# Performance work log

Hardware: AMD Instinct MI355X
Metric: run time of the kernel (lower is better)

Reference implementation:

```python
import jax, jax.numpy as jnp
import numpy as np

B, S, D = 2, 2048, 1024
H, HD = 16, 64  # num_heads, head_dim
EPS = 1e-6      # flax LayerNorm default
ROPE_BASE = 10000.0


def _layernorm(x, scale, bias=None, eps=EPS):
    mu = jnp.mean(x, axis=-1, keepdims=True)
    var = jnp.mean(jnp.square(x - mu), axis=-1, keepdims=True)
    y = (x - mu) * jax.lax.rsqrt(var + eps) * scale
    return y + bias if bias is not None else y


def _rotate_half(x):
    x1, x2 = x[..., : x.shape[-1] // 2], x[..., x.shape[-1] // 2 :]
    return jnp.concatenate((-x2, x1), axis=-1)


def _rope_tables(seq_len, head_dim, dtype):
    inv_freq = 1.0 / ROPE_BASE ** (jnp.arange(0, head_dim, 2, dtype=jnp.float32) / head_dim)
    t = jnp.arange(seq_len, dtype=jnp.float32)
    freqs = jnp.einsum('i,j->ij', t, inv_freq)          # [S, HD/2]
    emb = jnp.concatenate((freqs, freqs), axis=-1)      # [S, HD]
    return jnp.cos(emb).astype(dtype), jnp.sin(emb).astype(dtype)


def setup_inputs() -> dict:
    key = jax.random.key(0)
    ks = jax.random.split(key, 4)
    return {
        'x': jax.random.normal(ks[0], (B, S, D), dtype=jnp.float32),
        'w_qkv': jax.random.normal(ks[1], (D, 3 * D), dtype=jnp.float32) * (1.0 / np.sqrt(D)),
        'b_qkv': jnp.zeros((3 * D,), dtype=jnp.float32),
        'w_out': jax.random.normal(ks[2], (D, D), dtype=jnp.float32) * (0.1 / np.sqrt(D)),
        'b_out': jnp.zeros((D,), dtype=jnp.float32),
        'ln_scale': jnp.ones((D,), dtype=jnp.float32),
        'ln_bias': jnp.zeros((D,), dtype=jnp.float32),
        'q_scale': jnp.ones((HD,), dtype=jnp.float32),
        'k_scale': jnp.ones((HD,), dtype=jnp.float32),
    }


def reference(x, w_qkv, b_qkv, w_out, b_out, ln_scale, ln_bias, q_scale, k_scale):
    b, s, d = x.shape
    # input LayerNorm
    xn = _layernorm(x, ln_scale, ln_bias)
    # fused QKV projection
    qkv = xn @ w_qkv + b_qkv                              # [B, S, 3D]
    q, k, v = jnp.split(qkv, 3, axis=-1)
    def to_bhsd(t):
        return t.reshape(b, s, H, HD).transpose(0, 2, 1, 3)
    q, k, v = to_bhsd(q), to_bhsd(k), to_bhsd(v)          # [B, H, S, HD]
    # per-head QK LayerNorm (no bias)
    q = _layernorm(q, q_scale)
    k = _layernorm(k, k_scale)
    # RoPE
    cos, sin = _rope_tables(s, HD, q.dtype)               # [S, HD]
    cos, sin = cos[None, None], sin[None, None]
    q = q * cos + _rotate_half(q) * sin
    k = k * cos + _rotate_half(k) * sin
    # scaled dot-product attention (softmax over key positions)
    scale = 1.0 / np.sqrt(HD)
    scores = jnp.einsum('bhqd,bhkd->bhqk', q, k) * scale  # [B, H, S, S]
    probs = jax.nn.softmax(scores, axis=-1)
    attn = jnp.einsum('bhqk,bhkd->bhqd', probs, v)        # [B, H, S, HD]
    attn = attn.transpose(0, 2, 1, 3).reshape(b, s, d)
    return attn @ w_out + b_out
```

## Files before the change

kernel.cpp:

```cpp
#include <hip/hip_runtime.h>
#include <math.h>

#define BB 2
#define SS 2048
#define DD 1024
#define HH 16
#define HDD 64
static constexpr float EPS = 1e-6f;

typedef __bf16 bf16x8 __attribute__((ext_vector_type(8)));
typedef __bf16 bf16x4 __attribute__((ext_vector_type(4)));
typedef float f32x4 __attribute__((ext_vector_type(4)));
typedef __attribute__((address_space(1))) const unsigned int gas_u32;
typedef __attribute__((address_space(3))) unsigned int las_u32;

__device__ __forceinline__ unsigned short f2bf(float f) {
    unsigned int u = __float_as_uint(f);
    u = (u + 0x7FFFu + ((u >> 16) & 1u)) >> 16;
    return (unsigned short)u;
}

__device__ __forceinline__ uint2 pack4bf(float a, float b, float c, float d) {
    bf16x4 v;
    v[0] = (__bf16)a; v[1] = (__bf16)b; v[2] = (__bf16)c; v[3] = (__bf16)d;
    return *(uint2*)&v;
}

__device__ __forceinline__ void async_ld16(const unsigned short* g, unsigned short* l) {
    __builtin_amdgcn_global_load_lds((gas_u32*)g, (las_u32*)l, 16, 0, 0);
}

__global__ __launch_bounds__(256) void cast_transpose(const float* __restrict__ w,
                                                      unsigned short* __restrict__ wt,
                                                      int K, int N) {
    __shared__ float tile[32][36];
    const int n0 = blockIdx.x * 32;
    const int k0 = blockIdx.y * 32;
    const int t = threadIdx.x;
    const int r = t >> 3;
    const int c = (t & 7) * 4;
    *(float4*)&tile[r][c] = *(const float4*)(w + (size_t)(k0 + r) * N + n0 + c);
    __syncthreads();
    unsigned short o[4];
#pragma unroll
    for (int i = 0; i < 4; i++) o[i] = f2bf(tile[c + i][r]);
    *(uint2*)(wt + (size_t)(n0 + r) * K + k0 + c) = *(uint2*)o;
}

__global__ __launch_bounds__(256) void ln_kernel(const float* __restrict__ x,
                                                 const float* __restrict__ scale,
                                                 const float* __restrict__ bias,
                                                 unsigned short* __restrict__ xn) {
    __shared__ float red[4];
    const int row = blockIdx.x;
    const int t = threadIdx.x;
    const float* xr = x + (size_t)row * DD + t * 4;

    float4 v = *(const float4*)xr;
    float s = v.x + v.y + v.z + v.w;
#pragma unroll
    for (int o = 32; o; o >>= 1) s += __shfl_xor(s, o);
    if ((t & 63) == 0) red[t >> 6] = s;
    __syncthreads();
    const float mu = (red[0] + red[1] + red[2] + red[3]) * (1.f / DD);

    float4 d = {v.x - mu, v.y - mu, v.z - mu, v.w - mu};
    float sq = d.x * d.x + d.y * d.y + d.z * d.z + d.w * d.w;
#pragma unroll
    for (int o = 32; o; o >>= 1) sq += __shfl_xor(sq, o);
    __syncthreads();
    if ((t & 63) == 0) red[t >> 6] = sq;
    __syncthreads();
    const float var = (red[0] + red[1] + red[2] + red[3]) * (1.f / DD);
    const float rstd = rsqrtf(var + EPS);

    const float4 sc = *(const float4*)(scale + t * 4);
    const float4 bi = *(const float4*)(bias + t * 4);
    unsigned short o[4];
    o[0] = f2bf(d.x * rstd * sc.x + bi.x);
    o[1] = f2bf(d.y * rstd * sc.y + bi.y);
    o[2] = f2bf(d.z * rstd * sc.z + bi.z);
    o[3] = f2bf(d.w * rstd * sc.w + bi.w);
    *(uint2*)(xn + (size_t)row * DD + t * 4) = *(uint2*)o;
}

__global__ __launch_bounds__(256) void gemm_mfma_bt(const unsigned short* __restrict__ A,
                                                    const unsigned short* __restrict__ Bt,
                                                    const float* __restrict__ bias,
                                                    float* __restrict__ C,
                                                    int M, int N, int K) {
    __shared__ __align__(16) unsigned short As[128][32];
    __shared__ __align__(16) unsigned short Bs[128][32];

    const int bm = blockIdx.y * 128;
    const int bn = blockIdx.x * 128;
    const int t = threadIdx.x;
    const int wv = t >> 6;
    const int ln = t & 63;
    const int m16 = ln & 15;
    const int quad = ln >> 4;
    const int wm = (wv >> 1) * 64;
    const int wn = (wv & 1) * 64;

    f32x4 acc[4][4];
#pragma unroll
    for (int i = 0; i < 4; i++)
#pragma unroll
        for (int j = 0; j < 4; j++) acc[i][j] = (f32x4){0.f, 0.f, 0.f, 0.f};

    const int srow = wv * 32 + (ln >> 2);
    const int sk = (ln & 3) * 8;
    const unsigned short* aptr = A + (size_t)(bm + srow) * K + sk;
    const unsigned short* bptr = Bt + (size_t)(bn + srow) * K + sk;
    unsigned short* al0 = &As[wv * 32][0];
    unsigned short* al1 = &As[wv * 32 + 16][0];
    unsigned short* bl0 = &Bs[wv * 32][0];
    unsigned short* bl1 = &Bs[wv * 32 + 16][0];

    for (int k0 = 0; k0 < K; k0 += 32) {
        __syncthreads();
        async_ld16(aptr, al0);
        async_ld16(aptr + 16 * (size_t)K, al1);
        async_ld16(bptr, bl0);
        async_ld16(bptr + 16 * (size_t)K, bl1);
        __syncthreads();

        bf16x8 af[4], bf[4];
#pragma unroll
        for (int i = 0; i < 4; i++)
            af[i] = *(const bf16x8*)&As[wm + i * 16 + m16][quad * 8];
#pragma unroll
        for (int j = 0; j < 4; j++)
            bf[j] = *(const bf16x8*)&Bs[wn + j * 16 + m16][quad * 8];
#pragma unroll
        for (int i = 0; i < 4; i++)
#pragma unroll
            for (int j = 0; j < 4; j++)
                acc[i][j] = __builtin_amdgcn_mfma_f32_16x16x32_bf16(af[i], bf[j], acc[i][j], 0, 0, 0);

        aptr += 32;
        bptr += 32;
    }

#pragma unroll
    for (int j = 0; j < 4; j++) {
        const int n = bn + wn + j * 16 + m16;
        const float bv = bias[n];
#pragma unroll
        for (int i = 0; i < 4; i++) {
            float* cp = C + (size_t)(bm + wm + i * 16 + quad * 4) * N + n;
#pragma unroll
            for (int r = 0; r < 4; r++)
                cp[(size_t)r * N] = acc[i][j][r] + bv;
        }
    }
}

__device__ __forceinline__ float wave_sum64(float x) {
#pragma unroll
    for (int o = 32; o; o >>= 1) x += __shfl_xor(x, o);
    return x;
}

__global__ __launch_bounds__(256) void head_ln_rope(const float* __restrict__ qkv,
                                                    const float* __restrict__ q_scale,
                                                    const float* __restrict__ k_scale,
                                                    unsigned short* __restrict__ qt,
                                                    unsigned short* __restrict__ kt,
                                                    unsigned short* __restrict__ vt) {
    const int wave = (blockIdx.x * 256 + threadIdx.x) >> 6;
    const int lane = threadIdx.x & 63;
    const int h = wave & (HH - 1);
    const int row = wave >> 4;
    const int b = row >> 11;
    const int s = row & (SS - 1);

    const float* base = qkv + (size_t)row * (3 * DD) + h * HDD;
    const float qv = base[lane];
    const float kv = base[DD + lane];
    const float vv = base[2 * DD + lane];

    const float mq = wave_sum64(qv) * (1.f / 64.f);
    const float dq = qv - mq;
    const float varq = wave_sum64(dq * dq) * (1.f / 64.f);
    const float yq = dq * rsqrtf(varq + EPS) * q_scale[lane];

    const float mk = wave_sum64(kv) * (1.f / 64.f);
    const float dk = kv - mk;
    const float vark = wave_sum64(dk * dk) * (1.f / 64.f);
    const float yk = dk * rsqrtf(vark + EPS) * k_scale[lane];

    const int i = lane & 31;
    const float ang = (float)s * exp2f(-(float)i * (13.287712379549449f / 32.f));
    const float cv = cosf(ang);
    const float sv = sinf(ang);
    const float pq = __shfl_xor(yq, 32);
    const float pk = __shfl_xor(yk, 32);
    const float rq = (lane < 32) ? -pq : pq;
    const float rk = (lane < 32) ? -pk : pk;
    const float oq = yq * cv + rq * sv;
    const float ok = yk * cv + rk * sv;

    const size_t oidx = (((size_t)(b * HH + h) * SS) + s) * HDD + lane;
    qt[oidx] = f2bf(oq * 0.18033688011112042f);
    kt[oidx] = f2bf(ok);
    vt[oidx] = f2bf(vv);
}

__global__ __launch_bounds__(256) void transpose_v(const unsigned short* __restrict__ vt,
                                                   unsigned short* __restrict__ vtT) {
    __shared__ unsigned short tile[64][72];
    const int bh = blockIdx.x >> 5;
    const int s0 = (blockIdx.x & 31) * 64;
    const int t = threadIdx.x;
    const int row = t >> 2;
    const int c0 = (t & 3) * 16;
    const unsigned short* src = vt + ((size_t)bh * SS + s0 + row) * HDD + c0;
    *(uint4*)&tile[row][c0]     = *(const uint4*)(src);
    *(uint4*)&tile[row][c0 + 8] = *(const uint4*)(src + 8);
    __syncthreads();
    unsigned short outv[16];
#pragma unroll
    for (int i = 0; i < 16; i++) outv[i] = tile[c0 + i][row];
    unsigned short* dst = vtT + ((size_t)bh * HDD + row) * SS + s0 + c0;
    *(uint4*)dst       = *(uint4*)&outv[0];
    *(uint4*)(dst + 8) = *(uint4*)&outv[8];
}

__global__ __launch_bounds__(256) void attn_mfma(const unsigned short* __restrict__ qt,
                                                 const unsigned short* __restrict__ kt,
                                                 const unsigned short* __restrict__ vtT,
                                                 unsigned short* __restrict__ attn) {
    __shared__ __align__(16) unsigned short Ks[64][72];
    __shared__ __align__(16) unsigned short Vs[64][72];
    __shared__ __align__(16) unsigned short Pb[4][32][72];

    const int bh = blockIdx.x >> 4;
    const int q0 = (blockIdx.x & 15) * 128;
    const int t = threadIdx.x;
    const int wq = t >> 6;
    const int lane = t & 63;
    const int m16 = lane & 15;
    const int quad = lane >> 4;

    bf16x8 qb[2][2];
#pragma unroll
    for (int u = 0; u < 2; u++) {
        const unsigned short* qp =
            qt + ((size_t)bh * SS + q0 + wq * 32 + u * 16 + m16) * HDD + quad * 8;
        qb[u][0] = *(const bf16x8*)qp;
        qb[u][1] = *(const bf16x8*)(qp + 32);
    }

    f32x4 O[2][4];
#pragma unroll
    for (int u = 0; u < 2; u++)
#pragma unroll
        for (int f = 0; f < 4; f++) O[u][f] = (f32x4){0.f, 0.f, 0.f, 0.f};
    float l[2] = {0.f, 0.f};

    const unsigned short* kbase = kt + (size_t)bh * SS * HDD;
    const unsigned short* vbase = vtT + (size_t)bh * HDD * SS;

    const int srow = t >> 2;
    const int sc0 = (t & 3) * 16;

    for (int k0 = 0; k0 < SS; k0 += 64) {
        __syncthreads();
        {
            const unsigned short* ksrc = kbase + (size_t)(k0 + srow) * HDD + sc0;
            *(uint4*)&Ks[srow][sc0]     = *(const uint4*)ksrc;
            *(uint4*)&Ks[srow][sc0 + 8] = *(const uint4*)(ksrc + 8);
            const unsigned short* vsrc = vbase + (size_t)srow * SS + k0 + sc0;
            *(uint4*)&Vs[srow][sc0]     = *(const uint4*)vsrc;
            *(uint4*)&Vs[srow][sc0 + 8] = *(const uint4*)(vsrc + 8);
        }
        __syncthreads();

        f32x4 S[2][4];
#pragma unroll
        for (int g = 0; g < 4; g++) {
            const bf16x8 ka0 = *(const bf16x8*)&Ks[g * 16 + m16][quad * 8];
            const bf16x8 ka1 = *(const bf16x8*)&Ks[g * 16 + m16][32 + quad * 8];
#pragma unroll
            for (int u = 0; u < 2; u++) {
                f32x4 a = (f32x4){0.f, 0.f, 0.f, 0.f};
                a = __builtin_amdgcn_mfma_f32_16x16x32_bf16(ka0, qb[u][0], a, 0, 0, 0);
                a = __builtin_amdgcn_mfma_f32_16x16x32_bf16(ka1, qb[u][1], a, 0, 0, 0);
                S[u][g] = a;
            }
        }

#pragma unroll
        for (int u = 0; u < 2; u++) {
#pragma unroll
            for (int g = 0; g < 4; g++) {
                const float p0 = exp2f(S[u][g][0] - 12.f);
                const float p1 = exp2f(S[u][g][1] - 12.f);
                const float p2 = exp2f(S[u][g][2] - 12.f);
                const float p3 = exp2f(S[u][g][3] - 12.f);
                l[u] += (p0 + p1) + (p2 + p3);
                *(uint2*)&Pb[wq][u * 16 + m16][g * 16 + quad * 4] = pack4bf(p0, p1, p2, p3);
            }
        }
        asm volatile("s_waitcnt lgkmcnt(0)" ::: "memory");

        bf16x8 pb[2][2];
#pragma unroll
        for (int u = 0; u < 2; u++) {
            pb[u][0] = *(const bf16x8*)&Pb[wq][u * 16 + m16][quad * 8];
            pb[u][1] = *(const bf16x8*)&Pb[wq][u * 16 + m16][32 + quad * 8];
        }

#pragma unroll
        for (int f = 0; f < 4; f++) {
            const bf16x8 va0 = *(const bf16x8*)&Vs[f * 16 + m16][quad * 8];
            const bf16x8 va1 = *(const bf16x8*)&Vs[f * 16 + m16][32 + quad * 8];
#pragma unroll
            for (int u = 0; u < 2; u++) {
                O[u][f] = __builtin_amdgcn_mfma_f32_16x16x32_bf16(va0, pb[u][0], O[u][f], 0, 0, 0);
                O[u][f] = __builtin_amdgcn_mfma_f32_16x16x32_bf16(va1, pb[u][1], O[u][f], 0, 0, 0);
            }
        }
    }

    const int b_ = bh >> 4;
    const int h_ = bh & 15;
#pragma unroll
    for (int u = 0; u < 2; u++) {
        float lt = l[u];
        lt += __shfl_xor(lt, 16);
        lt += __shfl_xor(lt, 32);
        const float inv = 1.f / lt;
        const int s_ = q0 + wq * 32 + u * 16 + m16;
        unsigned short* orow = attn + ((size_t)b_ * SS + s_) * DD + h_ * HDD;
#pragma unroll
        for (int f = 0; f < 4; f++) {
            *(uint2*)(orow + f * 16 + quad * 4) =
                pack4bf(O[u][f][0] * inv, O[u][f][1] * inv, O[u][f][2] * inv, O[u][f][3] * inv);
        }
    }
}

extern "C" void kernel_launch(void* const* d_in, const int* in_sizes, int n_in,
                              void* d_out, int out_size, void* d_ws, size_t ws_size,
                              hipStream_t stream) {
    const float* x        = (const float*)d_in[0];
    const float* w_qkv    = (const float*)d_in[1];
    const float* b_qkv    = (const float*)d_in[2];
    const float* w_out    = (const float*)d_in[3];
    const float* b_out    = (const float*)d_in[4];
    const float* ln_scale = (const float*)d_in[5];
    const float* ln_bias  = (const float*)d_in[6];
    const float* q_scale  = (const float*)d_in[7];
    const float* k_scale  = (const float*)d_in[8];
    float* out = (float*)d_out;

    char* ws = (char*)d_ws;
    const size_t MB = 1024 * 1024;
    unsigned short* xn    = (unsigned short*)(ws + 0);
    float*          qkv   = (float*)(ws + 16 * MB);
    unsigned short* wqkvT = (unsigned short*)(ws + 64 * MB);
    unsigned short* woutT = (unsigned short*)(ws + 70 * MB);
    unsigned short* qt    = (unsigned short*)(ws + 72 * MB);
    unsigned short* kt    = (unsigned short*)(ws + 80 * MB);
    unsigned short* vt    = (unsigned short*)(ws + 88 * MB);
    unsigned short* vtT   = (unsigned short*)(ws + 96 * MB);
    unsigned short* attn  = (unsigned short*)(ws + 104 * MB);

    const int M = BB * SS;

    cast_transpose<<<dim3(3 * DD / 32, DD / 32), 256, 0, stream>>>(w_qkv, wqkvT, DD, 3 * DD);
    cast_transpose<<<dim3(DD / 32, DD / 32), 256, 0, stream>>>(w_out, woutT, DD, DD);

    ln_kernel<<<M, 256, 0, stream>>>(x, ln_scale, ln_bias, xn);

    gemm_mfma_bt<<<dim3(3 * DD / 128, M / 128), 256, 0, stream>>>(xn, wqkvT, b_qkv, qkv,
                                                                  M, 3 * DD, DD);

    head_ln_rope<<<M * HH / 4, 256, 0, stream>>>(qkv, q_scale, k_scale, qt, kt, vt);

    transpose_v<<<BB * HH * (SS / 64), 256, 0, stream>>>(vt, vtT);

    attn_mfma<<<BB * HH * (SS / 128), 256, 0, stream>>>(qt, kt, vtT, attn);

    gemm_mfma_bt<<<dim3(DD / 128, M / 128), 256, 0, stream>>>(attn, woutT, b_out, out,
                                                              M, DD, DD);
}
```

Measured before the change: 263.1 us.

## Split attention over key halves, swizzle LDS, and precompute RoPE tables

```diff
diff --git a/kernel.cpp b/kernel.cpp
--- a/kernel.cpp
+++ b/kernel.cpp
@@ -45,6 +45,16 @@
 #pragma unroll
     for (int i = 0; i < 4; i++) o[i] = f2bf(tile[c + i][r]);
     *(uint2*)(wt + (size_t)(n0 + r) * K + k0 + c) = *(uint2*)o;
+}
+
+__global__ __launch_bounds__(256) void rope_tables(float* __restrict__ ctab,
+                                                   float* __restrict__ stab) {
+    const int idx = blockIdx.x * 256 + threadIdx.x;
+    const int s = idx >> 5;
+    const int i = idx & 31;
+    const float ang = (float)s * exp2f(-(float)i * (13.287712379549449f / 32.f));
+    ctab[idx] = cosf(ang);
+    stab[idx] = sinf(ang);
 }
 
 __global__ __launch_bounds__(256) void ln_kernel(const float* __restrict__ x,
@@ -165,6 +175,8 @@
 __global__ __launch_bounds__(256) void head_ln_rope(const float* __restrict__ qkv,
                                                     const float* __restrict__ q_scale,
                                                     const float* __restrict__ k_scale,
+                                                    const float* __restrict__ ctab,
+                                                    const float* __restrict__ stab,
                                                     unsigned short* __restrict__ qt,
                                                     unsigned short* __restrict__ kt,
                                                     unsigned short* __restrict__ vt) {
@@ -191,9 +203,8 @@
     const float yk = dk * rsqrtf(vark + EPS) * k_scale[lane];
 
     const int i = lane & 31;
-    const float ang = (float)s * exp2f(-(float)i * (13.287712379549449f / 32.f));
-    const float cv = cosf(ang);
-    const float sv = sinf(ang);
+    const float cv = ctab[s * 32 + i];
+    const float sv = stab[s * 32 + i];
     const float pq = __shfl_xor(yq, 32);
     const float pk = __shfl_xor(yk, 32);
     const float rq = (lane < 32) ? -pq : pq;
@@ -227,21 +238,33 @@
     *(uint4*)(dst + 8) = *(uint4*)&outv[8];
 }
 
-__global__ __launch_bounds__(256) void attn_mfma(const unsigned short* __restrict__ qt,
-                                                 const unsigned short* __restrict__ kt,
-                                                 const unsigned short* __restrict__ vtT,
-                                                 unsigned short* __restrict__ attn) {
-    __shared__ __align__(16) unsigned short Ks[64][72];
-    __shared__ __align__(16) unsigned short Vs[64][72];
-    __shared__ __align__(16) unsigned short Pb[4][32][72];
+__global__ __launch_bounds__(256, 4) void attn_mfma(const unsigned short* __restrict__ qt,
+                                                    const unsigned short* __restrict__ kt,
+                                                    const unsigned short* __restrict__ vtT,
+                                                    float* __restrict__ Opart,
+                                                    float* __restrict__ lpart) {
+    __shared__ __align__(16) unsigned short KsS[64 * 64];
+    __shared__ __align__(16) unsigned short VsS[64 * 64];
+    __shared__ __align__(16) unsigned short PbS[4][32 * 64];
 
     const int bh = blockIdx.x >> 4;
     const int q0 = (blockIdx.x & 15) * 128;
+    const int ks = blockIdx.y;
     const int t = threadIdx.x;
     const int wq = t >> 6;
     const int lane = t & 63;
     const int m16 = lane & 15;
     const int quad = lane >> 4;
+    const int m7 = m16 & 7;
+
+    const int cs = quad ^ m7;
+    const int koff = m16 * 64 + cs * 8;
+    const int srow = t >> 2;
+    const int sch = (t & 3) * 2;
+    const int sw0 = srow * 64 + ((sch)     ^ (srow & 7)) * 8;
+    const int sw1 = srow * 64 + ((sch + 1) ^ (srow & 7)) * 8;
+    const int pwb = m16 * 64 + 4 * (quad & 1);
+    const int qh = quad >> 1;
 
     bf16x8 qb[2][2];
 #pragma unroll
@@ -252,40 +275,42 @@
         qb[u][1] = *(const bf16x8*)(qp + 32);
     }
 
+    bf16x8 ones;
+#pragma unroll
+    for (int j = 0; j < 8; j++) ones[j] = (__bf16)1.0f;
+
     f32x4 O[2][4];
 #pragma unroll
     for (int u = 0; u < 2; u++)
 #pragma unroll
         for (int f = 0; f < 4; f++) O[u][f] = (f32x4){0.f, 0.f, 0.f, 0.f};
-    float l[2] = {0.f, 0.f};
+    f32x4 lacc[2] = {(f32x4){0.f, 0.f, 0.f, 0.f}, (f32x4){0.f, 0.f, 0.f, 0.f}};
 
     const unsigned short* kbase = kt + (size_t)bh * SS * HDD;
     const unsigned short* vbase = vtT + (size_t)bh * HDD * SS;
-
-    const int srow = t >> 2;
-    const int sc0 = (t & 3) * 16;
-
-    for (int k0 = 0; k0 < SS; k0 += 64) {
+    const f32x4 cinit = (f32x4){-12.f, -12.f, -12.f, -12.f};
+
+    const int kstart = ks * (SS / 2);
+    for (int k0 = kstart; k0 < kstart + SS / 2; k0 += 64) {
         __syncthreads();
         {
-            const unsigned short* ksrc = kbase + (size_t)(k0 + srow) * HDD + sc0;
-            *(uint4*)&Ks[srow][sc0]     = *(const uint4*)ksrc;
-            *(uint4*)&Ks[srow][sc0 + 8] = *(const uint4*)(ksrc + 8);
-            const unsigned short* vsrc = vbase + (size_t)srow * SS + k0 + sc0;
-            *(uint4*)&Vs[srow][sc0]     = *(const uint4*)vsrc;
-            *(uint4*)&Vs[srow][sc0 + 8] = *(const uint4*)(vsrc + 8);
+            const unsigned short* ksrc = kbase + (size_t)(k0 + srow) * HDD + sch * 8;
+            *(uint4*)&KsS[sw0] = *(const uint4*)ksrc;
+            *(uint4*)&KsS[sw1] = *(const uint4*)(ksrc + 8);
+            const unsigned short* vsrc = vbase + (size_t)srow * SS + k0 + sch * 8;
+            *(uint4*)&VsS[sw0] = *(const uint4*)vsrc;
+            *(uint4*)&VsS[sw1] = *(const uint4*)(vsrc + 8);
         }
         __syncthreads();
 
         f32x4 S[2][4];
 #pragma unroll
         for (int g = 0; g < 4; g++) {
-            const bf16x8 ka0 = *(const bf16x8*)&Ks[g * 16 + m16][quad * 8];
-            const bf16x8 ka1 = *(const bf16x8*)&Ks[g * 16 + m16][32 + quad * 8];
+            const bf16x8 ka0 = *(const bf16x8*)&KsS[g * 1024 + koff];
+            const bf16x8 ka1 = *(const bf16x8*)&KsS[g * 1024 + (koff ^ 32)];
 #pragma unroll
             for (int u = 0; u < 2; u++) {
-                f32x4 a = (f32x4){0.f, 0.f, 0.f, 0.f};
-                a = __builtin_amdgcn_mfma_f32_16x16x32_bf16(ka0, qb[u][0], a, 0, 0, 0);
+                f32x4 a = __builtin_amdgcn_mfma_f32_16x16x32_bf16(ka0, qb[u][0], cinit, 0, 0, 0);
                 a = __builtin_amdgcn_mfma_f32_16x16x32_bf16(ka1, qb[u][1], a, 0, 0, 0);
                 S[u][g] = a;
             }
@@ -295,12 +320,12 @@
         for (int u = 0; u < 2; u++) {
 #pragma unroll
             for (int g = 0; g < 4; g++) {
-                const float p0 = exp2f(S[u][g][0] - 12.f);
-                const float p1 = exp2f(S[u][g][1] - 12.f);
-                const float p2 = exp2f(S[u][g][2] - 12.f);
-                const float p3 = exp2f(S[u][g][3] - 12.f);
-                l[u] += (p0 + p1) + (p2 + p3);
-                *(uint2*)&Pb[wq][u * 16 + m16][g * 16 + quad * 4] = pack4bf(p0, p1, p2, p3);
+                const float p0 = exp2f(S[u][g][0]);
+                const float p1 = exp2f(S[u][g][1]);
+                const float p2 = exp2f(S[u][g][2]);
+                const float p3 = exp2f(S[u][g][3]);
+                *(uint2*)&PbS[wq][u * 1024 + pwb + ((2 * g + qh) ^ m7) * 8] =
+                    pack4bf(p0, p1, p2, p3);
             }
         }
         asm volatile("s_waitcnt lgkmcnt(0)" ::: "memory");
@@ -308,14 +333,19 @@
         bf16x8 pb[2][2];
 #pragma unroll
         for (int u = 0; u < 2; u++) {
-            pb[u][0] = *(const bf16x8*)&Pb[wq][u * 16 + m16][quad * 8];
-            pb[u][1] = *(const bf16x8*)&Pb[wq][u * 16 + m16][32 + quad * 8];
-        }
-
+            pb[u][0] = *(const bf16x8*)&PbS[wq][u * 1024 + koff];
+            pb[u][1] = *(const bf16x8*)&PbS[wq][u * 1024 + (koff ^ 32)];
+        }
+
+#pragma unroll
+        for (int u = 0; u < 2; u++) {
+            lacc[u] = __builtin_amdgcn_mfma_f32_16x16x32_bf16(ones, pb[u][0], lacc[u], 0, 0, 0);
+            lacc[u] = __builtin_amdgcn_mfma_f32_16x16x32_bf16(ones, pb[u][1], lacc[u], 0, 0, 0);
+        }
 #pragma unroll
         for (int f = 0; f < 4; f++) {
-            const bf16x8 va0 = *(const bf16x8*)&Vs[f * 16 + m16][quad * 8];
-            const bf16x8 va1 = *(const bf16x8*)&Vs[f * 16 + m16][32 + quad * 8];
+            const bf16x8 va0 = *(const bf16x8*)&VsS[f * 1024 + koff];
+            const bf16x8 va1 = *(const bf16x8*)&VsS[f * 1024 + (koff ^ 32)];
 #pragma unroll
             for (int u = 0; u < 2; u++) {
                 O[u][f] = __builtin_amdgcn_mfma_f32_16x16x32_bf16(va0, pb[u][0], O[u][f], 0, 0, 0);
@@ -326,20 +356,37 @@
 
     const int b_ = bh >> 4;
     const int h_ = bh & 15;
+    float* obase0 = Opart + (size_t)ks * ((size_t)BB * SS * DD);
 #pragma unroll
     for (int u = 0; u < 2; u++) {
-        float lt = l[u];
-        lt += __shfl_xor(lt, 16);
-        lt += __shfl_xor(lt, 32);
-        const float inv = 1.f / lt;
         const int s_ = q0 + wq * 32 + u * 16 + m16;
-        unsigned short* orow = attn + ((size_t)b_ * SS + s_) * DD + h_ * HDD;
-#pragma unroll
-        for (int f = 0; f < 4; f++) {
-            *(uint2*)(orow + f * 16 + quad * 4) =
-                pack4bf(O[u][f][0] * inv, O[u][f][1] * inv, O[u][f][2] * inv, O[u][f][3] * inv);
-        }
+        float* orow = obase0 + ((size_t)b_ * SS + s_) * DD + h_ * HDD;
+#pragma unroll
+        for (int f = 0; f < 4; f++)
+            *(f32x4*)(orow + f * 16 + quad * 4) = O[u][f];
+        if (quad == 0)
+            lpart[ks * (32 * SS) + bh * SS + s_] = lacc[u][0];
     }
+}
+
+__global__ __launch_bounds__(256) void combine_attn(const float* __restrict__ Opart,
+                                                    const float* __restrict__ lpart,
+                                                    unsigned short* __restrict__ attn) {
+    const int row = blockIdx.x;
+    const int t = threadIdx.x;
+    const int c = t * 4;
+    const int h = t >> 4;
+    const int b = row >> 11;
+    const int s = row & (SS - 1);
+
+    const size_t off = (size_t)row * DD + c;
+    const float4 o0 = *(const float4*)(Opart + off);
+    const float4 o1 = *(const float4*)(Opart + (size_t)BB * SS * DD + off);
+    const int li = (b * HH + h) * SS + s;
+    const float inv = 1.f / (lpart[li] + lpart[32 * SS + li]);
+
+    *(uint2*)(attn + off) = pack4bf((o0.x + o1.x) * inv, (o0.y + o1.y) * inv,
+                                    (o0.z + o1.z) * inv, (o0.w + o1.w) * inv);
 }
 
 extern "C" void kernel_launch(void* const* d_in, const int* in_sizes, int n_in,
@@ -359,7 +406,11 @@
     char* ws = (char*)d_ws;
     const size_t MB = 1024 * 1024;
     unsigned short* xn    = (unsigned short*)(ws + 0);
+    float*          lpart = (float*)(ws + 8 * MB);
+    float*          ctab  = (float*)(ws + 9 * MB);
+    float*          stab  = (float*)(ws + 10 * MB);
     float*          qkv   = (float*)(ws + 16 * MB);
+    float*          Opart = (float*)(ws + 16 * MB);
     unsigned short* wqkvT = (unsigned short*)(ws + 64 * MB);
     unsigned short* woutT = (unsigned short*)(ws + 70 * MB);
     unsigned short* qt    = (unsigned short*)(ws + 72 * MB);
@@ -372,17 +423,21 @@
 
     cast_transpose<<<dim3(3 * DD / 32, DD / 32), 256, 0, stream>>>(w_qkv, wqkvT, DD, 3 * DD);
     cast_transpose<<<dim3(DD / 32, DD / 32), 256, 0, stream>>>(w_out, woutT, DD, DD);
+    rope_tables<<<SS * 32 / 256, 256, 0, stream>>>(ctab, stab);
 
     ln_kernel<<<M, 256, 0, stream>>>(x, ln_scale, ln_bias, xn);
 
     gemm_mfma_bt<<<dim3(3 * DD / 128, M / 128), 256, 0, stream>>>(xn, wqkvT, b_qkv, qkv,
                                                                   M, 3 * DD, DD);
 
-    head_ln_rope<<<M * HH / 4, 256, 0, stream>>>(qkv, q_scale, k_scale, qt, kt, vt);
+    head_ln_rope<<<M * HH / 4, 256, 0, stream>>>(qkv, q_scale, k_scale, ctab, stab,
+                                                 qt, kt, vt);
 
     transpose_v<<<BB * HH * (SS / 64), 256, 0, stream>>>(vt, vtT);
 
-    attn_mfma<<<BB * HH * (SS / 128), 256, 0, stream>>>(qt, kt, vtT, attn);
+    attn_mfma<<<dim3(BB * HH * (SS / 128), 2), 256, 0, stream>>>(qt, kt, vtT, Opart, lpart);
+
+    combine_attn<<<M, 256, 0, stream>>>(Opart, lpart, attn);
 
     gemm_mfma_bt<<<dim3(DD / 128, M / 128), 256, 0, stream>>>(attn, woutT, b_out, out,
                                                               M, DD, DD);
```

Result: faster. 251.9 us (-4.3%).
